# Kernel tuning notes

Hardware: AMD Instinct MI355X
Metric: run time of the kernel (lower is better)

Reference implementation:

```python
import jax, jax.numpy as jnp
import numpy as np

SIZE = 512
NUM_NODES = 32
BATCH = 8192
EPS = 1e-5  # torch LayerNorm default eps


def setup_inputs() -> dict:
    key = jax.random.key(0)
    k1, k2 = jax.random.split(key)
    x = jax.random.normal(k1, (BATCH, NUM_NODES), dtype=jnp.float32)
    # xavier_uniform_ for Linear(1, SIZE): bound = sqrt(6/(1+SIZE))
    bound = float(np.sqrt(6.0 / (1 + SIZE)))
    w = jax.random.uniform(k2, (SIZE,), dtype=jnp.float32, minval=-bound, maxval=bound)
    b = jnp.zeros((SIZE,), dtype=jnp.float32)
    gamma = jnp.ones((SIZE,), dtype=jnp.float32)
    beta = jnp.zeros((SIZE,), dtype=jnp.float32)
    return {"x": x, "w": w, "b": b, "gamma": gamma, "beta": beta}


def reference(x, w, b, gamma, beta):
    scale = jnp.sqrt(jnp.asarray(SIZE, dtype=x.dtype))
    # Broadcast scalar->vector projection (collapses the per-node python loop)
    # h: (batch, num_nodes, size)
    h = (x[:, :, None] * w + b) * scale
    # LayerNorm over the last dim (biased variance, like torch.nn.LayerNorm)
    mean = jnp.mean(h, axis=-1, keepdims=True)
    var = jnp.mean(jnp.square(h - mean), axis=-1, keepdims=True)
    out = (h - mean) * jax.lax.rsqrt(var + EPS) * gamma + beta
    # dropout is identity in eval mode
    return out
```

## Files before the change

kernel.cpp:

```cpp
#include <hip/hip_runtime.h>

#define LN_SIZE 512
#define LN_NODES 32
#define LN_BATCH 8192
#define LN_ROWS (LN_BATCH * LN_NODES)
#define LN_EPS 1e-5f
#define LN_SCALE 22.62741699796952f
#define LN_ROWS_PER_WAVE 32

__global__ __launch_bounds__(LN_SIZE) void ln_pre_kernel(
    const float* __restrict__ w, const float* __restrict__ b,
    const float* __restrict__ gamma, float* __restrict__ ws) {
  __shared__ float sh[LN_SIZE];
  const int j = threadIdx.x;
  const float wj = w[j];
  const float bj = b[j];
  const float gj = gamma[j];

  auto bsum = [&](float v) -> float {
    __syncthreads();
    sh[j] = v;
    __syncthreads();
    for (int off = LN_SIZE / 2; off > 0; off >>= 1) {
      if (j < off) sh[j] += sh[j + off];
      __syncthreads();
    }
    return sh[0];
  };

  const float inv_n = 1.0f / (float)LN_SIZE;
  const float mw = bsum(wj) * inv_n;
  const float mb = bsum(bj) * inv_n;
  const float dw = wj - mw;
  const float db = bj - mb;
  const float Sww = bsum(dw * dw) * inv_n;
  const float Swb = bsum(dw * db) * inv_n;
  const float Sbb = bsum(db * db) * inv_n;

  ws[j]            = dw * gj;
  ws[LN_SIZE + j]  = db * gj;
  if (j == 0) {
    const float s2 = (float)LN_SIZE;
    ws[2 * LN_SIZE + 0] = s2 * Sww;
    ws[2 * LN_SIZE + 1] = 2.0f * s2 * Swb;
    ws[2 * LN_SIZE + 2] = s2 * Sbb;
  }
}

__global__ __launch_bounds__(256) void ln_main_kernel(
    const float* __restrict__ x, const float* __restrict__ ws,
    const float* __restrict__ beta, float* __restrict__ out) {
  const int wid  = (int)((blockIdx.x * blockDim.x + threadIdx.x) >> 6);
  const int lane = (int)(threadIdx.x & 63);
  const int j    = lane * 8;

  const float4 a0 = *(const float4*)(ws + j);
  const float4 a1 = *(const float4*)(ws + j + 4);
  const float4 b0 = *(const float4*)(ws + LN_SIZE + j);
  const float4 b1 = *(const float4*)(ws + LN_SIZE + j + 4);
  const float4 g0 = *(const float4*)(beta + j);
  const float4 g1 = *(const float4*)(beta + j + 4);
  const float c2 = ws[2 * LN_SIZE + 0];
  const float c1 = ws[2 * LN_SIZE + 1];
  const float c0 = ws[2 * LN_SIZE + 2];

  const int row0 = wid * LN_ROWS_PER_WAVE;
  if (row0 >= LN_ROWS) return;

  const float xv  = x[row0 + (lane & 31)];
  const float var = fmaf(fmaf(c2, xv, c1), xv, c0);
  const float rv  = LN_SCALE * rsqrtf(var + LN_EPS);

  float* dst = out + (size_t)row0 * LN_SIZE + j;
#pragma unroll
  for (int i = 0; i < LN_ROWS_PER_WAVE; ++i) {
    const float xi = __shfl(xv, i);
    const float ri = __shfl(rv, i);

    float4 o0, o1;
    o0.x = fmaf(fmaf(xi, a0.x, b0.x), ri, g0.x);
    o0.y = fmaf(fmaf(xi, a0.y, b0.y), ri, g0.y);
    o0.z = fmaf(fmaf(xi, a0.z, b0.z), ri, g0.z);
    o0.w = fmaf(fmaf(xi, a0.w, b0.w), ri, g0.w);
    o1.x = fmaf(fmaf(xi, a1.x, b1.x), ri, g1.x);
    o1.y = fmaf(fmaf(xi, a1.y, b1.y), ri, g1.y);
    o1.z = fmaf(fmaf(xi, a1.z, b1.z), ri, g1.z);
    o1.w = fmaf(fmaf(xi, a1.w, b1.w), ri, g1.w);

    *(float4*)(dst)     = o0;
    *(float4*)(dst + 4) = o1;
    dst += LN_SIZE;
  }
}

extern "C" void kernel_launch(void* const* d_in, const int* in_sizes, int n_in,
                              void* d_out, int out_size, void* d_ws, size_t ws_size,
                              hipStream_t stream) {
  const float* x     = (const float*)d_in[0];
  const float* w     = (const float*)d_in[1];
  const float* b     = (const float*)d_in[2];
  const float* gamma = (const float*)d_in[3];
  const float* beta  = (const float*)d_in[4];
  float* out = (float*)d_out;
  float* ws  = (float*)d_ws;

  ln_pre_kernel<<<1, LN_SIZE, 0, stream>>>(w, b, gamma, ws);
  ln_main_kernel<<<2048, 256, 0, stream>>>(x, ws, beta, out);
}
```

Before: 111.0 us.

## Fuse precompute into main LayerNorm kernel and use nontemporal stores

Removes the separate single-block precompute kernel: every block now recomputes the w/b statistics with wave shuffles plus a small shared-memory reduction, and derives the centered, gamma-scaled coefficients itself. This drops one kernel launch and the serialized dependency on a tiny one-block kernel. It also switches the output writes to nontemporal stores to reduce cache pollution on the 512 MB write stream. The trade-offs are redundant reduction work in all 2048 blocks, and variance computed as E[x²]−mean², which is less numerically robust.

After: 251.9 us. +127.0%, slower.

```diff
diff --git a/kernel.cpp b/kernel.cpp
--- a/kernel.cpp
+++ b/kernel.cpp
@@ -1,70 +1,84 @@
 #include <hip/hip_runtime.h>
 
 #define LN_SIZE 512
-#define LN_NODES 32
-#define LN_BATCH 8192
-#define LN_ROWS (LN_BATCH * LN_NODES)
+#define LN_ROWS (8192 * 32)
 #define LN_EPS 1e-5f
 #define LN_SCALE 22.62741699796952f
-#define LN_ROWS_PER_WAVE 32
+#define RPW 32
 
-__global__ __launch_bounds__(LN_SIZE) void ln_pre_kernel(
-    const float* __restrict__ w, const float* __restrict__ b,
-    const float* __restrict__ gamma, float* __restrict__ ws) {
-  __shared__ float sh[LN_SIZE];
-  const int j = threadIdx.x;
-  const float wj = w[j];
-  const float bj = b[j];
-  const float gj = gamma[j];
+typedef float f32x4 __attribute__((ext_vector_type(4)));
 
-  auto bsum = [&](float v) -> float {
-    __syncthreads();
-    sh[j] = v;
-    __syncthreads();
-    for (int off = LN_SIZE / 2; off > 0; off >>= 1) {
-      if (j < off) sh[j] += sh[j + off];
-      __syncthreads();
-    }
-    return sh[0];
-  };
+__global__ __launch_bounds__(256) void ln_fused_kernel(
+    const float* __restrict__ x, const float* __restrict__ w,
+    const float* __restrict__ b, const float* __restrict__ gamma,
+    const float* __restrict__ beta, float* __restrict__ out) {
+  const int tid  = (int)threadIdx.x;
+  const int lane = tid & 63;
+  const int wv   = tid >> 6;
+
+  float sw, sb, sww, swb, sbb;
+  {
+    const int j0 = tid, j1 = tid + 256;
+    const float w0 = w[j0], w1 = w[j1];
+    const float p0 = b[j0], p1 = b[j1];
+    sw  = w0 + w1;
+    sb  = p0 + p1;
+    sww = w0 * w0 + w1 * w1;
+    swb = w0 * p0 + w1 * p1;
+    sbb = p0 * p0 + p1 * p1;
+  }
+#pragma unroll
+  for (int off = 32; off > 0; off >>= 1) {
+    sw  += __shfl_xor(sw, off);
+    sb  += __shfl_xor(sb, off);
+    sww += __shfl_xor(sww, off);
+    swb += __shfl_xor(swb, off);
+    sbb += __shfl_xor(sbb, off);
+  }
+  __shared__ float red[4][5];
+  if (lane == 0) {
+    red[wv][0] = sw; red[wv][1] = sb; red[wv][2] = sww;
+    red[wv][3] = swb; red[wv][4] = sbb;
+  }
+  __syncthreads();
+  sw  = red[0][0] + red[1][0] + red[2][0] + red[3][0];
+  sb  = red[0][1] + red[1][1] + red[2][1] + red[3][1];
+  sww = red[0][2] + red[1][2] + red[2][2] + red[3][2];
+  swb = red[0][3] + red[1][3] + red[2][3] + red[3][3];
+  sbb = red[0][4] + red[1][4] + red[2][4] + red[3][4];
 
   const float inv_n = 1.0f / (float)LN_SIZE;
-  const float mw = bsum(wj) * inv_n;
-  const float mb = bsum(bj) * inv_n;
-  const float dw = wj - mw;
-  const float db = bj - mb;
-  const float Sww = bsum(dw * dw) * inv_n;
-  const float Swb = bsum(dw * db) * inv_n;
-  const float Sbb = bsum(db * db) * inv_n;
+  const float mw  = sw * inv_n;
+  const float mb  = sb * inv_n;
+  const float Sww = sww * inv_n - mw * mw;
+  const float Swb = swb * inv_n - mw * mb;
+  const float Sbb = sbb * inv_n - mb * mb;
+  const float c2 = (float)LN_SIZE * Sww;
+  const float c1 = 2.0f * (float)LN_SIZE * Swb;
+  const float c0 = (float)LN_SIZE * Sbb;
 
-  ws[j]            = dw * gj;
-  ws[LN_SIZE + j]  = db * gj;
-  if (j == 0) {
-    const float s2 = (float)LN_SIZE;
-    ws[2 * LN_SIZE + 0] = s2 * Sww;
-    ws[2 * LN_SIZE + 1] = 2.0f * s2 * Swb;
-    ws[2 * LN_SIZE + 2] = s2 * Sbb;
-  }
-}
+  const int j = lane * 8;
+  const float4 wv0 = *(const float4*)(w + j);
+  const float4 wv1 = *(const float4*)(w + j + 4);
+  const float4 bv0 = *(const float4*)(b + j);
+  const float4 bv1 = *(const float4*)(b + j + 4);
+  const float4 gv0 = *(const float4*)(gamma + j);
+  const float4 gv1 = *(const float4*)(gamma + j + 4);
+  const float4 g0  = *(const float4*)(beta + j);
+  const float4 g1  = *(const float4*)(beta + j + 4);
 
-__global__ __launch_bounds__(256) void ln_main_kernel(
-    const float* __restrict__ x, const float* __restrict__ ws,
-    const float* __restrict__ beta, float* __restrict__ out) {
-  const int wid  = (int)((blockIdx.x * blockDim.x + threadIdx.x) >> 6);
-  const int lane = (int)(threadIdx.x & 63);
-  const int j    = lane * 8;
+  float4 a0, a1, B0, B1;
+  a0.x = (wv0.x - mw) * gv0.x;  a0.y = (wv0.y - mw) * gv0.y;
+  a0.z = (wv0.z - mw) * gv0.z;  a0.w = (wv0.w - mw) * gv0.w;
+  a1.x = (wv1.x - mw) * gv1.x;  a1.y = (wv1.y - mw) * gv1.y;
+  a1.z = (wv1.z - mw) * gv1.z;  a1.w = (wv1.w - mw) * gv1.w;
+  B0.x = (bv0.x - mb) * gv0.x;  B0.y = (bv0.y - mb) * gv0.y;
+  B0.z = (bv0.z - mb) * gv0.z;  B0.w = (bv0.w - mb) * gv0.w;
+  B1.x = (bv1.x - mb) * gv1.x;  B1.y = (bv1.y - mb) * gv1.y;
+  B1.z = (bv1.z - mb) * gv1.z;  B1.w = (bv1.w - mb) * gv1.w;
 
-  const float4 a0 = *(const float4*)(ws + j);
-  const float4 a1 = *(const float4*)(ws + j + 4);
-  const float4 b0 = *(const float4*)(ws + LN_SIZE + j);
-  const float4 b1 = *(const float4*)(ws + LN_SIZE + j + 4);
-  const float4 g0 = *(const float4*)(beta + j);
-  const float4 g1 = *(const float4*)(beta + j + 4);
-  const float c2 = ws[2 * LN_SIZE + 0];
-  const float c1 = ws[2 * LN_SIZE + 1];
-  const float c0 = ws[2 * LN_SIZE + 2];
-
-  const int row0 = wid * LN_ROWS_PER_WAVE;
+  const int wid  = (int)((blockIdx.x * blockDim.x + tid) >> 6);
+  const int row0 = wid * RPW;
   if (row0 >= LN_ROWS) return;
 
   const float xv  = x[row0 + (lane & 31)];
@@ -73,22 +87,22 @@
 
   float* dst = out + (size_t)row0 * LN_SIZE + j;
 #pragma unroll
-  for (int i = 0; i < LN_ROWS_PER_WAVE; ++i) {
+  for (int i = 0; i < RPW; ++i) {
     const float xi = __shfl(xv, i);
     const float ri = __shfl(rv, i);
 
-    float4 o0, o1;
-    o0.x = fmaf(fmaf(xi, a0.x, b0.x), ri, g0.x);
-    o0.y = fmaf(fmaf(xi, a0.y, b0.y), ri, g0.y);
-    o0.z = fmaf(fmaf(xi, a0.z, b0.z), ri, g0.z);
-    o0.w = fmaf(fmaf(xi, a0.w, b0.w), ri, g0.w);
-    o1.x = fmaf(fmaf(xi, a1.x, b1.x), ri, g1.x);
-    o1.y = fmaf(fmaf(xi, a1.y, b1.y), ri, g1.y);
-    o1.z = fmaf(fmaf(xi, a1.z, b1.z), ri, g1.z);
-    o1.w = fmaf(fmaf(xi, a1.w, b1.w), ri, g1.w);
+    f32x4 o0, o1;
+    o0.x = fmaf(fmaf(xi, a0.x, B0.x), ri, g0.x);
+    o0.y = fmaf(fmaf(xi, a0.y, B0.y), ri, g0.y);
+    o0.z = fmaf(fmaf(xi, a0.z, B0.z), ri, g0.z);
+    o0.w = fmaf(fmaf(xi, a0.w, B0.w), ri, g0.w);
+    o1.x = fmaf(fmaf(xi, a1.x, B1.x), ri, g1.x);
+    o1.y = fmaf(fmaf(xi, a1.y, B1.y), ri, g1.y);
+    o1.z = fmaf(fmaf(xi, a1.z, B1.z), ri, g1.z);
+    o1.w = fmaf(fmaf(xi, a1.w, B1.w), ri, g1.w);
 
-    *(float4*)(dst)     = o0;
-    *(float4*)(dst + 4) = o1;
+    __builtin_nontemporal_store(o0, (f32x4*)dst);
+    __builtin_nontemporal_store(o1, (f32x4*)(dst + 4));
     dst += LN_SIZE;
   }
 }
@@ -102,8 +116,7 @@
   const float* gamma = (const float*)d_in[3];
   const float* beta  = (const float*)d_in[4];
   float* out = (float*)d_out;
-  float* ws  = (float*)d_ws;
+  (void)d_ws; (void)ws_size;
 
-  ln_pre_kernel<<<1, LN_SIZE, 0, stream>>>(w, b, gamma, ws);
-  ln_main_kernel<<<2048, 256, 0, stream>>>(x, ws, beta, out);
+  ln_fused_kernel<<<2048, 256, 0, stream>>>(x, w, b, gamma, beta, out);
 }
```
